# Optimization experiments

Hardware: AMD Instinct MI355X
Metric: run time of the kernel (lower is better)

Reference implementation:

```python
import jax, jax.numpy as jnp
import numpy as np

B, C, D, H, W = 4, 64, 64, 64, 64
EPS = 1e-5

def setup_inputs() -> dict:
    key = jax.random.key(0)
    ks = jax.random.split(key, 10)
    s = 1.0 / np.sqrt(C)
    so = 1.0 / np.sqrt(D)
    return {
        "x": jax.random.normal(ks[0], (B, C, H, W), jnp.float32),
        "gn_weight": jnp.ones((C,), jnp.float32),
        "gn_bias": jnp.zeros((C,), jnp.float32),
        "wq": jax.random.uniform(ks[1], (D, C), jnp.float32, -s, s),
        "bq": jax.random.uniform(ks[2], (D,), jnp.float32, -s, s),
        "wk": jax.random.uniform(ks[3], (D, C), jnp.float32, -s, s),
        "bk": jax.random.uniform(ks[4], (D,), jnp.float32, -s, s),
        "wv": jax.random.uniform(ks[5], (D, C), jnp.float32, -s, s),
        "bv": jax.random.uniform(ks[6], (D,), jnp.float32, -s, s),
        "wo": jax.random.uniform(ks[7], (D, D), jnp.float32, -so, so),
        "bo": jax.random.uniform(ks[8], (D,), jnp.float32, -so, so),
    }

def reference(x, gn_weight, gn_bias, wq, bq, wk, bk, wv, bv, wo, bo):
    # GroupNorm with num_groups == channels: per (batch, channel) norm over H,W
    mu = jnp.mean(x, axis=(2, 3), keepdims=True)
    var = jnp.var(x, axis=(2, 3), keepdims=True)
    xn = (x - mu) * jax.lax.rsqrt(var + EPS)
    xn = xn * gn_weight[None, :, None, None] + gn_bias[None, :, None, None]

    # 1x1 convs == channel matmuls; flatten spatial: bcn
    xf = xn.reshape(B, C, H * W)
    Q = jnp.einsum('dc,bcn->bdn', wq, xf) + bq[None, :, None]
    K = jnp.einsum('dc,bcn->bdn', wk, xf) + bk[None, :, None]
    V = jnp.einsum('dc,bcn->bdn', wv, xf) + bv[None, :, None]

    scale = 1.0 / jnp.sqrt(jnp.asarray(D, x.dtype))
    aff = jnp.einsum('bdn,bdm->bnm', Q, K) * scale  # [B, N, N]
    aff = jax.nn.softmax(aff, axis=2)
    att = jnp.einsum('bnm,bdm->bdn', aff, V)  # [B, D, N]

    out = jnp.einsum('ed,bdn->ben', wo, att) + bo[None, :, None]
    return out.reshape(B, D, H, W)
```

## Files before the change

kernel.cpp:

```cpp
#include <hip/hip_runtime.h>


#define B_ 4
#define C_ 64
#define D_ 64
#define N_ 4096

using bf16x8 = __attribute__((ext_vector_type(8))) short;
using u16x8  = __attribute__((ext_vector_type(8))) unsigned short;
using u32x4  = __attribute__((ext_vector_type(4))) unsigned int;
using f32x16 = __attribute__((ext_vector_type(16))) float;
using h16x8  = __attribute__((ext_vector_type(8))) _Float16;

__device__ __forceinline__ unsigned short f2bf(float f) {
    unsigned u = __builtin_bit_cast(unsigned, f);
    u = (u + 0x7FFFu + ((u >> 16) & 1u)) >> 16;
    return (unsigned short)u;
}

__device__ __forceinline__ void gload16(const void* g, void* l) {
    __builtin_amdgcn_global_load_lds(
        (const __attribute__((address_space(1))) unsigned int*)g,
        (__attribute__((address_space(3))) unsigned int*)l, 16, 0, 0);
}

__global__ __launch_bounds__(1024)
void gn_stats_kernel(const float* __restrict__ x, float* __restrict__ stats) {
    __shared__ float red[32];
    const int bx  = blockIdx.x;
    const int tid = threadIdx.x;
    const float4* xp = (const float4*)(x + (size_t)bx * N_);
    float4 v = xp[tid];
    float s = (v.x + v.y) + (v.z + v.w);
    float q = (v.x * v.x + v.y * v.y) + (v.z * v.z + v.w * v.w);
#pragma unroll
    for (int off = 1; off < 64; off <<= 1) {
        s += __shfl_xor(s, off);
        q += __shfl_xor(q, off);
    }
    const int w = tid >> 6;
    if ((tid & 63) == 0) { red[w * 2] = s; red[w * 2 + 1] = q; }
    __syncthreads();
    if (w == 0) {
        const int lane = tid & 63;
        float sl = (lane < 16) ? red[lane * 2] : 0.f;
        float ql = (lane < 16) ? red[lane * 2 + 1] : 0.f;
#pragma unroll
        for (int off = 1; off < 16; off <<= 1) {
            sl += __shfl_xor(sl, off);
            ql += __shfl_xor(ql, off);
        }
        if (lane == 0) {
            float mu  = sl * (1.f / 4096.f);
            float var = ql * (1.f / 4096.f) - mu * mu;
            var = fmaxf(var, 0.f);
            stats[bx * 2]     = mu;
            stats[bx * 2 + 1] = 1.f / sqrtf(var + 1e-5f);
        }
    }
}

__global__ __launch_bounds__(512)
void gn_qkv_kernel(const float* __restrict__ x, const float* __restrict__ stats,
                   const float* __restrict__ gnw, const float* __restrict__ gnb,
                   const float* __restrict__ wq, const float* __restrict__ bq,
                   const float* __restrict__ wk, const float* __restrict__ bk,
                   const float* __restrict__ wv, const float* __restrict__ bv,
                   unsigned short* __restrict__ Qt, unsigned short* __restrict__ Kf,
                   unsigned short* __restrict__ Vf) {
    __shared__ float xn[64 * 64];
    __shared__ __align__(16) char vs[64 * 128];
    const int t  = threadIdx.x;
    const int bx = blockIdx.x;
    const int b  = bx >> 6;
    const int n0 = (bx & 63) * 64;

    {
        const int c  = t >> 3;
        const int nc = (t & 7) * 8;
        const float* xp = x + (size_t)(b * 64 + c) * N_ + n0 + nc;
        float4 xa = *(const float4*)(xp);
        float4 xb = *(const float4*)(xp + 4);
        float mu = stats[(b * 64 + c) * 2];
        float rs = stats[(b * 64 + c) * 2 + 1];
        float gw = gnw[c] * rs;
        float gb = gnb[c] - mu * gw;
        float* xr = xn + c * 64 + nc;
        xr[0] = xa.x * gw + gb; xr[1] = xa.y * gw + gb;
        xr[2] = xa.z * gw + gb; xr[3] = xa.w * gw + gb;
        xr[4] = xb.x * gw + gb; xr[5] = xb.y * gw + gb;
        xr[6] = xb.z * gw + gb; xr[7] = xb.w * gw + gb;
    }
    __syncthreads();

    const int n    = t & 63;
    const int dblk = __builtin_amdgcn_readfirstlane(t >> 6);
    const int d0   = dblk * 8;

    float aq[8], ak[8], av[8];
#pragma unroll
    for (int i = 0; i < 8; ++i) { aq[i] = 0.f; ak[i] = 0.f; av[i] = 0.f; }

#pragma unroll 4
    for (int c = 0; c < 64; ++c) {
        const float xv = xn[c * 64 + n];
#pragma unroll
        for (int i = 0; i < 8; ++i) {
            aq[i] += wq[(d0 + i) * 64 + c] * xv;
            ak[i] += wk[(d0 + i) * 64 + c] * xv;
            av[i] += wv[(d0 + i) * 64 + c] * xv;
        }
    }

    const float QS = 0.18033688011112042f;
    const int m = n0 + n;
    u16x8 qv, kv, vb;
#pragma unroll
    for (int i = 0; i < 8; ++i) {
        qv[i] = f2bf((aq[i] + bq[d0 + i]) * QS);
        kv[i] = f2bf(ak[i] + bk[d0 + i]);
        vb[i] = f2bf(av[i] + bv[d0 + i]);
    }
    *(u16x8*)(Qt + ((size_t)(b * N_ + m)) * 64 + d0) = qv;
    {
        const int kc = dblk >> 1, h = dblk & 1, mt = m >> 5;
        *(u16x8*)(Kf + ((size_t)((b * 128 + mt) * 4 + kc)) * 512
                     + (h * 32 + (m & 31)) * 8) = kv;
    }
    *(u16x8*)(vs + n * 128 + ((dblk * 16) ^ ((n & 7) << 4))) = vb;
    __syncthreads();

    {
        const int mc_l = t >> 7;
        const int dt   = (t >> 6) & 1;
        const int lp   = t & 63;
        const int hp   = lp >> 5;
        const int dcol = (lp & 31) + dt * 32;
        const int cbase = (dcol & ~7) * 2;
        const int clow  = (dcol & 7) * 2;
        u16x8 tmp;
#pragma unroll
        for (int j = 0; j < 8; ++j) {
            const int ml = mc_l * 16 + hp * 8 + j;
            tmp[j] = *(const unsigned short*)(
                vs + ml * 128 + (cbase ^ (j << 4)) + clow);
        }
        *(u16x8*)(Vf + ((size_t)((b * 256 + (n0 >> 4) + mc_l) * 2 + dt)) * 512
                     + lp * 8) = tmp;
    }
}

__global__ __launch_bounds__(256, 4)
void attn_kernel(const unsigned short* __restrict__ Qt,
                 const unsigned short* __restrict__ Kf,
                 const unsigned short* __restrict__ Vf,
                 _Float16* __restrict__ Opart, float* __restrict__ Lpart,
                 int mspan) {
    __shared__ __align__(16) char smem[2 * 16384];
    const int tid  = threadIdx.x;
    const int lane = tid & 63;
    const int wvu  = __builtin_amdgcn_readfirstlane(tid >> 6);
    const int c    = lane & 31;
    const int h    = lane >> 5;
    const int bid  = blockIdx.x;
    const int b    = bid & 3;
    const int t2   = bid >> 2;
    const int qb   = t2 & 31;
    const int s    = t2 >> 5;
    const int qg0  = qb * 128 + wvu * 32;

    const unsigned short* qp = Qt + (size_t)(b * N_ + qg0 + c) * 64 + h * 8;
    bf16x8 qa[4];
#pragma unroll
    for (int kc = 0; kc < 4; ++kc) qa[kc] = *(const bf16x8*)(qp + kc * 16);

    f32x16 oacc0, oacc1;
#pragma unroll
    for (int i = 0; i < 16; ++i) { oacc0[i] = 0.f; oacc1[i] = 0.f; }
    float lsum = 0.f;

    const char* kfB = (const char*)Kf + (size_t)b * 524288;
    const char* vfB = (const char*)Vf + (size_t)b * 524288;
    const int   lof = lane * 16;

    const int NT = mspan >> 6;
    const int mstart = s * mspan;

    {
        const char* kT = kfB + (size_t)(mstart >> 5) * 4096;
        const char* vT = vfB + (size_t)(mstart >> 4) * 2048;
        gload16(kT + (wvu    ) * 1024 + lof, smem + (wvu    ) * 1024);
        gload16(kT + (wvu + 4) * 1024 + lof, smem + (wvu + 4) * 1024);
        gload16(vT + (wvu    ) * 1024 + lof, smem + 8192 + (wvu    ) * 1024);
        gload16(vT + (wvu + 4) * 1024 + lof, smem + 8192 + (wvu + 4) * 1024);
    }
    __syncthreads();

    for (int t = 0; t < NT; ++t) {
        char* buf = smem + ((t & 1) ? 16384 : 0);
        if (t + 1 < NT) {
            const int mn = mstart + (t + 1) * 64;
            const char* kT = kfB + (size_t)(mn >> 5) * 4096;
            const char* vT = vfB + (size_t)(mn >> 4) * 2048;
            char* dst = smem + ((t & 1) ? 0 : 16384);
            gload16(kT + (wvu    ) * 1024 + lof, dst + (wvu    ) * 1024);
            gload16(kT + (wvu + 4) * 1024 + lof, dst + (wvu + 4) * 1024);
            gload16(vT + (wvu    ) * 1024 + lof, dst + 8192 + (wvu    ) * 1024);
            gload16(vT + (wvu + 4) * 1024 + lof, dst + 8192 + (wvu + 4) * 1024);
        }

#pragma unroll
        for (int g = 0; g < 2; ++g) {
            const char* kb = buf + g * 4096 + lof;
            bf16x8 kf0 = *(const bf16x8*)(kb);
            bf16x8 kf1 = *(const bf16x8*)(kb + 1024);
            bf16x8 kf2 = *(const bf16x8*)(kb + 2048);
            bf16x8 kf3 = *(const bf16x8*)(kb + 3072);
            f32x16 sa;
#pragma unroll
            for (int i = 0; i < 16; ++i) sa[i] = 0.f;
            __builtin_amdgcn_s_setprio(1);
            sa = __builtin_amdgcn_mfma_f32_32x32x16_bf16(kf0, qa[0], sa, 0, 0, 0);
            sa = __builtin_amdgcn_mfma_f32_32x32x16_bf16(kf1, qa[1], sa, 0, 0, 0);
            sa = __builtin_amdgcn_mfma_f32_32x32x16_bf16(kf2, qa[2], sa, 0, 0, 0);
            sa = __builtin_amdgcn_mfma_f32_32x32x16_bf16(kf3, qa[3], sa, 0, 0, 0);
            __builtin_amdgcn_s_setprio(0);
#pragma unroll
            for (int i = 0; i < 16; ++i) {
                float pv = exp2f(sa[i]);
                sa[i] = pv;
                lsum += pv;
            }
            unsigned dw[8];
#pragma unroll
            for (int i = 0; i < 8; ++i)
                asm("v_cvt_pk_bf16_f32 %0, %1, %2"
                    : "=v"(dw[i]) : "v"(sa[2 * i]), "v"(sa[2 * i + 1]));
            asm("v_permlane32_swap_b32 %0, %1" : "+v"(dw[0]), "+v"(dw[2]));
            asm("v_permlane32_swap_b32 %0, %1" : "+v"(dw[1]), "+v"(dw[3]));
            asm("v_permlane32_swap_b32 %0, %1" : "+v"(dw[4]), "+v"(dw[6]));
            asm("v_permlane32_swap_b32 %0, %1" : "+v"(dw[5]), "+v"(dw[7]));
            bf16x8 pf0 = __builtin_bit_cast(bf16x8, (u32x4){dw[0], dw[1], dw[2], dw[3]});
            bf16x8 pf1 = __builtin_bit_cast(bf16x8, (u32x4){dw[4], dw[5], dw[6], dw[7]});

            const char* vb = buf + 8192 + g * 4096 + lof;
            bf16x8 vf0 = *(const bf16x8*)(vb);
            bf16x8 vf1 = *(const bf16x8*)(vb + 1024);
            bf16x8 vf2 = *(const bf16x8*)(vb + 2048);
            bf16x8 vf3 = *(const bf16x8*)(vb + 3072);
            __builtin_amdgcn_s_setprio(1);
            oacc0 = __builtin_amdgcn_mfma_f32_32x32x16_bf16(vf0, pf0, oacc0, 0, 0, 0);
            oacc1 = __builtin_amdgcn_mfma_f32_32x32x16_bf16(vf1, pf0, oacc1, 0, 0, 0);
            oacc0 = __builtin_amdgcn_mfma_f32_32x32x16_bf16(vf2, pf1, oacc0, 0, 0, 0);
            oacc1 = __builtin_amdgcn_mfma_f32_32x32x16_bf16(vf3, pf1, oacc1, 0, 0, 0);
            __builtin_amdgcn_s_setprio(0);
        }

        __syncthreads();
    }

    float rs = lsum + __shfl_xor(lsum, 32);

    const size_t s4b = (size_t)(s * 4 + b);
    _Float16* ob = Opart + (s4b * 64 << 12);
#pragma unroll
    for (int r = 0; r < 16; ++r) {
        const int row = (r & 3) + 8 * (r >> 2) + 4 * h;
        ob[((size_t)row << 12) + qg0 + c]        = (_Float16)oacc0[r];
        ob[((size_t)(row + 32) << 12) + qg0 + c] = (_Float16)oacc1[r];
    }
    if (h == 0)
        Lpart[(s4b << 12) + qg0 + c] = rs;
}

__global__ __launch_bounds__(256)
void out_proj_kernel(const _Float16* __restrict__ Opart, const float* __restrict__ Lpart,
                     const float* __restrict__ wo, const float* __restrict__ bo,
                     float* __restrict__ out, int S) {
    __shared__ float invl[32];
    __shared__ float attm[64 * 33];
    const int t  = threadIdx.x;
    const int bx = blockIdx.x;
    const int b  = bx >> 7;
    const int n0 = (bx & 127) * 32;

    if (t < 32) {
        float sum = 0.f;
        for (int s = 0; s < S; ++s)
            sum += Lpart[(((size_t)(s * 4 + b)) << 12) + n0 + t];
        invl[t] = 1.f / sum;
    }
    __syncthreads();

    {
        const int d  = t >> 2;
        const int nb = (t & 3) * 8;
        float o[8] = {0.f, 0.f, 0.f, 0.f, 0.f, 0.f, 0.f, 0.f};
        for (int s = 0; s < S; ++s) {
            h16x8 v = *(const h16x8*)(
                Opart + (((size_t)((s * 4 + b) * 64 + d)) << 12) + n0 + nb);
#pragma unroll
            for (int j = 0; j < 8; ++j) o[j] += (float)v[j];
        }
#pragma unroll
        for (int j = 0; j < 8; ++j)
            attm[d * 33 + nb + j] = o[j] * invl[nb + j];
    }
    __syncthreads();

    const int nn = t & 31;
    const int e0 = (t >> 5) * 8;
    float acc[8];
#pragma unroll
    for (int i = 0; i < 8; ++i) acc[i] = bo[e0 + i];
#pragma unroll 8
    for (int d = 0; d < 64; ++d) {
        const float xv = attm[d * 33 + nn];
#pragma unroll
        for (int i = 0; i < 8; ++i) acc[i] += wo[(e0 + i) * 64 + d] * xv;
    }
#pragma unroll
    for (int i = 0; i < 8; ++i)
        out[((size_t)(b * 64 + e0 + i) << 12) + n0 + nn] = acc[i];
}

extern "C" void kernel_launch(void* const* d_in, const int* in_sizes, int n_in,
                              void* d_out, int out_size, void* d_ws, size_t ws_size,
                              hipStream_t stream) {
    const float* x   = (const float*)d_in[0];
    const float* gnw = (const float*)d_in[1];
    const float* gnb = (const float*)d_in[2];
    const float* wq  = (const float*)d_in[3];
    const float* bq  = (const float*)d_in[4];
    const float* wk  = (const float*)d_in[5];
    const float* bk  = (const float*)d_in[6];
    const float* wv  = (const float*)d_in[7];
    const float* bv  = (const float*)d_in[8];
    const float* wo  = (const float*)d_in[9];
    const float* bo  = (const float*)d_in[10];
    float* out = (float*)d_out;

    char* wsb = (char*)d_ws;
    float*          stats = (float*)wsb;
    unsigned short* Qt    = (unsigned short*)(wsb + 2048);
    unsigned short* Kf    = (unsigned short*)(wsb + 2048 + 2097152);
    unsigned short* Vf    = (unsigned short*)(wsb + 2048 + 2 * 2097152);

    const size_t base = 2048 + 3ull * 2097152;
    auto need = [&](int S) {
        return base + (size_t)S * (65536 + 2097152);
    };
    const int S = (ws_size >= need(8)) ? 8
                : (ws_size >= need(4)) ? 4
                : (ws_size >= need(2)) ? 2 : 1;
    const int mspan = N_ / S;
    float*    Lpart = (float*)(wsb + base);
    _Float16* Opart = (_Float16*)(wsb + base + (size_t)S * 65536);

    gn_stats_kernel<<<dim3(B_ * C_), dim3(1024), 0, stream>>>(x, stats);
    gn_qkv_kernel<<<dim3(B_ * 64), dim3(512), 0, stream>>>(
        x, stats, gnw, gnb, wq, bq, wk, bk, wv, bv, Qt, Kf, Vf);
    attn_kernel<<<dim3(128 * S), dim3(256), 0, stream>>>(
        Qt, Kf, Vf, Opart, Lpart, mspan);
    out_proj_kernel<<<dim3(B_ * 128), dim3(256), 0, stream>>>(
        Opart, Lpart, wo, bo, out, S);
}
```

Measured before the change: 69.73 us.

## Fuse all four stages into one persistent cooperative kernel with grid syncs

Replaces the four separate launches (GN stats, GN+QKV projection, attention, output projection) with a single cooperative persistent kernel. Each phase loops over virtual blocks and is separated from the next by grid.sync(). The QKV stage is retiled to 16-column chunks with float4 weight loads so that it fits 256 threads. This removes launch gaps and inter-kernel drains, at the cost of grid-barrier overhead, smaller QKV tiles and occupancy tied to the attention phase's resource needs.

```diff
diff --git a/kernel.cpp b/kernel.cpp
--- a/kernel.cpp
+++ b/kernel.cpp
@@ -1,4 +1,7 @@
 #include <hip/hip_runtime.h>
+#include <hip/hip_cooperative_groups.h>
+
+namespace cg = cooperative_groups;
 
 
 #define B_ 4
@@ -7,6 +10,7 @@
 #define N_ 4096
 
 using bf16x8 = __attribute__((ext_vector_type(8))) short;
+using u16x4  = __attribute__((ext_vector_type(4))) unsigned short;
 using u16x8  = __attribute__((ext_vector_type(8))) unsigned short;
 using u32x4  = __attribute__((ext_vector_type(4))) unsigned int;
 using f32x16 = __attribute__((ext_vector_type(16))) float;
@@ -24,304 +28,306 @@
         (__attribute__((address_space(3))) unsigned int*)l, 16, 0, 0);
 }
 
-__global__ __launch_bounds__(1024)
-void gn_stats_kernel(const float* __restrict__ x, float* __restrict__ stats) {
-    __shared__ float red[32];
-    const int bx  = blockIdx.x;
+__global__ __launch_bounds__(256, 4)
+void fused_kernel(const float* __restrict__ x, const float* __restrict__ gnw,
+                  const float* __restrict__ gnb, const float* __restrict__ wq,
+                  const float* __restrict__ bq, const float* __restrict__ wk,
+                  const float* __restrict__ bk, const float* __restrict__ wv,
+                  const float* __restrict__ bv, const float* __restrict__ wo,
+                  const float* __restrict__ bo, float* __restrict__ out,
+                  float* __restrict__ stats, unsigned short* __restrict__ Qt,
+                  unsigned short* __restrict__ Kf, unsigned short* __restrict__ Vf,
+                  _Float16* __restrict__ Opart, float* __restrict__ Lpart,
+                  int S, int mspan) {
+    __shared__ __align__(16) char smem[32768];
+    cg::grid_group grid = cg::this_grid();
     const int tid = threadIdx.x;
-    const float4* xp = (const float4*)(x + (size_t)bx * N_);
-    float4 v = xp[tid];
-    float s = (v.x + v.y) + (v.z + v.w);
-    float q = (v.x * v.x + v.y * v.y) + (v.z * v.z + v.w * v.w);
-#pragma unroll
-    for (int off = 1; off < 64; off <<= 1) {
-        s += __shfl_xor(s, off);
-        q += __shfl_xor(q, off);
-    }
-    const int w = tid >> 6;
-    if ((tid & 63) == 0) { red[w * 2] = s; red[w * 2 + 1] = q; }
-    __syncthreads();
-    if (w == 0) {
-        const int lane = tid & 63;
-        float sl = (lane < 16) ? red[lane * 2] : 0.f;
-        float ql = (lane < 16) ? red[lane * 2 + 1] : 0.f;
-#pragma unroll
-        for (int off = 1; off < 16; off <<= 1) {
-            sl += __shfl_xor(sl, off);
-            ql += __shfl_xor(ql, off);
-        }
-        if (lane == 0) {
-            float mu  = sl * (1.f / 4096.f);
-            float var = ql * (1.f / 4096.f) - mu * mu;
-            var = fmaxf(var, 0.f);
-            stats[bx * 2]     = mu;
-            stats[bx * 2 + 1] = 1.f / sqrtf(var + 1e-5f);
+    const int G   = gridDim.x;
+    const int bid = blockIdx.x;
+
+    {
+        float* red = (float*)smem;
+        for (int vb = bid; vb < B_ * C_; vb += G) {
+            const float4* xp = (const float4*)(x + (size_t)vb * N_);
+            float s = 0.f, q = 0.f;
+#pragma unroll
+            for (int r = 0; r < 4; ++r) {
+                float4 v = xp[r * 256 + tid];
+                s += (v.x + v.y) + (v.z + v.w);
+                q += (v.x * v.x + v.y * v.y) + (v.z * v.z + v.w * v.w);
+            }
+#pragma unroll
+            for (int off = 1; off < 64; off <<= 1) {
+                s += __shfl_xor(s, off);
+                q += __shfl_xor(q, off);
+            }
+            const int w = tid >> 6;
+            if ((tid & 63) == 0) { red[w * 2] = s; red[w * 2 + 1] = q; }
+            __syncthreads();
+            if (tid == 0) {
+                float Sm = red[0] + red[2] + red[4] + red[6];
+                float Qm = red[1] + red[3] + red[5] + red[7];
+                float mu  = Sm * (1.f / 4096.f);
+                float var = Qm * (1.f / 4096.f) - mu * mu;
+                var = fmaxf(var, 0.f);
+                stats[vb * 2]     = mu;
+                stats[vb * 2 + 1] = 1.f / sqrtf(var + 1e-5f);
+            }
+            __syncthreads();
         }
     }
-}
-
-__global__ __launch_bounds__(512)
-void gn_qkv_kernel(const float* __restrict__ x, const float* __restrict__ stats,
-                   const float* __restrict__ gnw, const float* __restrict__ gnb,
-                   const float* __restrict__ wq, const float* __restrict__ bq,
-                   const float* __restrict__ wk, const float* __restrict__ bk,
-                   const float* __restrict__ wv, const float* __restrict__ bv,
-                   unsigned short* __restrict__ Qt, unsigned short* __restrict__ Kf,
-                   unsigned short* __restrict__ Vf) {
-    __shared__ float xn[64 * 64];
-    __shared__ __align__(16) char vs[64 * 128];
-    const int t  = threadIdx.x;
-    const int bx = blockIdx.x;
-    const int b  = bx >> 6;
-    const int n0 = (bx & 63) * 64;
+    grid.sync();
 
     {
-        const int c  = t >> 3;
-        const int nc = (t & 7) * 8;
-        const float* xp = x + (size_t)(b * 64 + c) * N_ + n0 + nc;
-        float4 xa = *(const float4*)(xp);
-        float4 xb = *(const float4*)(xp + 4);
-        float mu = stats[(b * 64 + c) * 2];
-        float rs = stats[(b * 64 + c) * 2 + 1];
-        float gw = gnw[c] * rs;
-        float gb = gnb[c] - mu * gw;
-        float* xr = xn + c * 64 + nc;
-        xr[0] = xa.x * gw + gb; xr[1] = xa.y * gw + gb;
-        xr[2] = xa.z * gw + gb; xr[3] = xa.w * gw + gb;
-        xr[4] = xb.x * gw + gb; xr[5] = xb.y * gw + gb;
-        xr[6] = xb.z * gw + gb; xr[7] = xb.w * gw + gb;
-    }
-    __syncthreads();
-
-    const int n    = t & 63;
-    const int dblk = __builtin_amdgcn_readfirstlane(t >> 6);
-    const int d0   = dblk * 8;
-
-    float aq[8], ak[8], av[8];
-#pragma unroll
-    for (int i = 0; i < 8; ++i) { aq[i] = 0.f; ak[i] = 0.f; av[i] = 0.f; }
-
+        float* xn = (float*)smem;
+        char*  vs = smem + 4096;
+        for (int vb = bid; vb < 1024; vb += G) {
+            const int b  = vb >> 8;
+            const int n0 = (vb & 255) * 16;
+            {
+                const int c = tid >> 2;
+                const int j = (tid & 3) * 4;
+                float4 xv = *(const float4*)(x + (size_t)(b * 64 + c) * N_ + n0 + j);
+                float mu = stats[(b * 64 + c) * 2];
+                float rs = stats[(b * 64 + c) * 2 + 1];
+                float gw = gnw[c] * rs;
+                float gb = gnb[c] - mu * gw;
+                xn[c * 16 + j + 0] = xv.x * gw + gb;
+                xn[c * 16 + j + 1] = xv.y * gw + gb;
+                xn[c * 16 + j + 2] = xv.z * gw + gb;
+                xn[c * 16 + j + 3] = xv.w * gw + gb;
+            }
+            __syncthreads();
+
+            const int n  = tid & 15;
+            const int d0 = (tid >> 4) * 4;
+            float aq[4] = {0.f, 0.f, 0.f, 0.f};
+            float ak[4] = {0.f, 0.f, 0.f, 0.f};
+            float av[4] = {0.f, 0.f, 0.f, 0.f};
 #pragma unroll 4
-    for (int c = 0; c < 64; ++c) {
-        const float xv = xn[c * 64 + n];
-#pragma unroll
-        for (int i = 0; i < 8; ++i) {
-            aq[i] += wq[(d0 + i) * 64 + c] * xv;
-            ak[i] += wk[(d0 + i) * 64 + c] * xv;
-            av[i] += wv[(d0 + i) * 64 + c] * xv;
+            for (int c4 = 0; c4 < 16; ++c4) {
+                float x0 = xn[(c4 * 4 + 0) * 16 + n];
+                float x1 = xn[(c4 * 4 + 1) * 16 + n];
+                float x2 = xn[(c4 * 4 + 2) * 16 + n];
+                float x3 = xn[(c4 * 4 + 3) * 16 + n];
+#pragma unroll
+                for (int i = 0; i < 4; ++i) {
+                    float4 wq4 = *(const float4*)(wq + (d0 + i) * 64 + c4 * 4);
+                    float4 wk4 = *(const float4*)(wk + (d0 + i) * 64 + c4 * 4);
+                    float4 wv4 = *(const float4*)(wv + (d0 + i) * 64 + c4 * 4);
+                    aq[i] += wq4.x * x0 + wq4.y * x1 + wq4.z * x2 + wq4.w * x3;
+                    ak[i] += wk4.x * x0 + wk4.y * x1 + wk4.z * x2 + wk4.w * x3;
+                    av[i] += wv4.x * x0 + wv4.y * x1 + wv4.z * x2 + wv4.w * x3;
+                }
+            }
+
+            const float QS = 0.18033688011112042f;
+            const int m = n0 + n;
+            u16x4 qv, kv, vv;
+#pragma unroll
+            for (int i = 0; i < 4; ++i) {
+                qv[i] = f2bf((aq[i] + bq[d0 + i]) * QS);
+                kv[i] = f2bf(ak[i] + bk[d0 + i]);
+                vv[i] = f2bf(av[i] + bv[d0 + i]);
+            }
+            *(u16x4*)(Qt + (size_t)(b * N_ + m) * 64 + d0) = qv;
+            {
+                const int kc = d0 >> 4, hk = (d0 >> 3) & 1, mt = m >> 5;
+                *(u16x4*)(Kf + ((size_t)((b * 128 + mt) * 4 + kc)) * 512
+                             + (hk * 32 + (m & 31)) * 8 + (d0 & 7)) = kv;
+            }
+            *(u16x4*)(vs + n * 128 + (((d0 >> 3) * 16) ^ ((n & 7) << 4))
+                         + (d0 & 7) * 2) = vv;
+            __syncthreads();
+
+            if (tid < 128) {
+                const int dt = tid >> 6;
+                const int lp = tid & 63;
+                const int hp = lp >> 5;
+                const int dcol  = (lp & 31) + dt * 32;
+                const int cbase = (dcol & ~7) * 2;
+                const int clow  = (dcol & 7) * 2;
+                u16x8 tmp;
+#pragma unroll
+                for (int j = 0; j < 8; ++j)
+                    tmp[j] = *(const unsigned short*)(
+                        vs + (hp * 8 + j) * 128 + (cbase ^ (j << 4)) + clow);
+                *(u16x8*)(Vf + ((size_t)((b * 256 + (n0 >> 4)) * 2 + dt)) * 512
+                             + lp * 8) = tmp;
+            }
+            __syncthreads();
         }
     }
-
-    const float QS = 0.18033688011112042f;
-    const int m = n0 + n;
-    u16x8 qv, kv, vb;
-#pragma unroll
-    for (int i = 0; i < 8; ++i) {
-        qv[i] = f2bf((aq[i] + bq[d0 + i]) * QS);
-        kv[i] = f2bf(ak[i] + bk[d0 + i]);
-        vb[i] = f2bf(av[i] + bv[d0 + i]);
+    grid.sync();
+
+    {
+        char* abuf = smem;
+        const int lane = tid & 63;
+        const int wvu  = __builtin_amdgcn_readfirstlane(tid >> 6);
+        const int c    = lane & 31;
+        const int h    = lane >> 5;
+        const int lof  = lane * 16;
+        const int nvb  = 128 * S;
+
+        for (int vb = bid; vb < nvb; vb += G) {
+            const int b   = vb & 3;
+            const int t2  = vb >> 2;
+            const int qb  = t2 & 31;
+            const int s   = t2 >> 5;
+            const int qg0 = qb * 128 + wvu * 32;
+
+            const unsigned short* qp = Qt + (size_t)(b * N_ + qg0 + c) * 64 + h * 8;
+            bf16x8 qa[4];
+#pragma unroll
+            for (int kc = 0; kc < 4; ++kc) qa[kc] = *(const bf16x8*)(qp + kc * 16);
+
+            f32x16 oacc0, oacc1;
+#pragma unroll
+            for (int i = 0; i < 16; ++i) { oacc0[i] = 0.f; oacc1[i] = 0.f; }
+            float lsum = 0.f;
+
+            const char* kfB = (const char*)Kf + (size_t)b * 524288;
+            const char* vfB = (const char*)Vf + (size_t)b * 524288;
+            const int NT = mspan >> 6;
+            const int mstart = s * mspan;
+
+            {
+                const char* kT = kfB + (size_t)(mstart >> 5) * 4096;
+                const char* vT = vfB + (size_t)(mstart >> 4) * 2048;
+                gload16(kT + (wvu    ) * 1024 + lof, abuf + (wvu    ) * 1024);
+                gload16(kT + (wvu + 4) * 1024 + lof, abuf + (wvu + 4) * 1024);
+                gload16(vT + (wvu    ) * 1024 + lof, abuf + 8192 + (wvu    ) * 1024);
+                gload16(vT + (wvu + 4) * 1024 + lof, abuf + 8192 + (wvu + 4) * 1024);
+            }
+            __syncthreads();
+
+            for (int t = 0; t < NT; ++t) {
+                char* buf = abuf + ((t & 1) ? 16384 : 0);
+                if (t + 1 < NT) {
+                    const int mn = mstart + (t + 1) * 64;
+                    const char* kT = kfB + (size_t)(mn >> 5) * 4096;
+                    const char* vT = vfB + (size_t)(mn >> 4) * 2048;
+                    char* dst = abuf + ((t & 1) ? 0 : 16384);
+                    gload16(kT + (wvu    ) * 1024 + lof, dst + (wvu    ) * 1024);
+                    gload16(kT + (wvu + 4) * 1024 + lof, dst + (wvu + 4) * 1024);
+                    gload16(vT + (wvu    ) * 1024 + lof, dst + 8192 + (wvu    ) * 1024);
+                    gload16(vT + (wvu + 4) * 1024 + lof, dst + 8192 + (wvu + 4) * 1024);
+                }
+
+#pragma unroll
+                for (int g = 0; g < 2; ++g) {
+                    const char* kb = buf + g * 4096 + lof;
+                    bf16x8 kf0 = *(const bf16x8*)(kb);
+                    bf16x8 kf1 = *(const bf16x8*)(kb + 1024);
+                    bf16x8 kf2 = *(const bf16x8*)(kb + 2048);
+                    bf16x8 kf3 = *(const bf16x8*)(kb + 3072);
+                    f32x16 sa;
+#pragma unroll
+                    for (int i = 0; i < 16; ++i) sa[i] = 0.f;
+                    __builtin_amdgcn_s_setprio(1);
+                    sa = __builtin_amdgcn_mfma_f32_32x32x16_bf16(kf0, qa[0], sa, 0, 0, 0);
+                    sa = __builtin_amdgcn_mfma_f32_32x32x16_bf16(kf1, qa[1], sa, 0, 0, 0);
+                    sa = __builtin_amdgcn_mfma_f32_32x32x16_bf16(kf2, qa[2], sa, 0, 0, 0);
+                    sa = __builtin_amdgcn_mfma_f32_32x32x16_bf16(kf3, qa[3], sa, 0, 0, 0);
+                    __builtin_amdgcn_s_setprio(0);
+#pragma unroll
+                    for (int i = 0; i < 16; ++i) {
+                        float pv = exp2f(sa[i]);
+                        sa[i] = pv;
+                        lsum += pv;
+                    }
+                    unsigned dw[8];
+#pragma unroll
+                    for (int i = 0; i < 8; ++i)
+                        asm("v_cvt_pk_bf16_f32 %0, %1, %2"
+                            : "=v"(dw[i]) : "v"(sa[2 * i]), "v"(sa[2 * i + 1]));
+                    asm("v_permlane32_swap_b32 %0, %1" : "+v"(dw[0]), "+v"(dw[2]));
+                    asm("v_permlane32_swap_b32 %0, %1" : "+v"(dw[1]), "+v"(dw[3]));
+                    asm("v_permlane32_swap_b32 %0, %1" : "+v"(dw[4]), "+v"(dw[6]));
+                    asm("v_permlane32_swap_b32 %0, %1" : "+v"(dw[5]), "+v"(dw[7]));
+                    bf16x8 pf0 = __builtin_bit_cast(bf16x8, (u32x4){dw[0], dw[1], dw[2], dw[3]});
+                    bf16x8 pf1 = __builtin_bit_cast(bf16x8, (u32x4){dw[4], dw[5], dw[6], dw[7]});
+
+                    const char* vbp = buf + 8192 + g * 4096 + lof;
+                    bf16x8 vf0 = *(const bf16x8*)(vbp);
+                    bf16x8 vf1 = *(const bf16x8*)(vbp + 1024);
+                    bf16x8 vf2 = *(const bf16x8*)(vbp + 2048);
+                    bf16x8 vf3 = *(const bf16x8*)(vbp + 3072);
+                    __builtin_amdgcn_s_setprio(1);
+                    oacc0 = __builtin_amdgcn_mfma_f32_32x32x16_bf16(vf0, pf0, oacc0, 0, 0, 0);
+                    oacc1 = __builtin_amdgcn_mfma_f32_32x32x16_bf16(vf1, pf0, oacc1, 0, 0, 0);
+                    oacc0 = __builtin_amdgcn_mfma_f32_32x32x16_bf16(vf2, pf1, oacc0, 0, 0, 0);
+                    oacc1 = __builtin_amdgcn_mfma_f32_32x32x16_bf16(vf3, pf1, oacc1, 0, 0, 0);
+                    __builtin_amdgcn_s_setprio(0);
+                }
+                __syncthreads();
+            }
+
+            float rs = lsum + __shfl_xor(lsum, 32);
+            const size_t s4b = (size_t)(s * 4 + b);
+            _Float16* ob = Opart + (s4b * 64 << 12);
+#pragma unroll
+            for (int r = 0; r < 16; ++r) {
+                const int row = (r & 3) + 8 * (r >> 2) + 4 * h;
+                ob[((size_t)row << 12) + qg0 + c]        = (_Float16)oacc0[r];
+                ob[((size_t)(row + 32) << 12) + qg0 + c] = (_Float16)oacc1[r];
+            }
+            if (h == 0)
+                Lpart[(s4b << 12) + qg0 + c] = rs;
+        }
     }
-    *(u16x8*)(Qt + ((size_t)(b * N_ + m)) * 64 + d0) = qv;
+    grid.sync();
+
     {
-        const int kc = dblk >> 1, h = dblk & 1, mt = m >> 5;
-        *(u16x8*)(Kf + ((size_t)((b * 128 + mt) * 4 + kc)) * 512
-                     + (h * 32 + (m & 31)) * 8) = kv;
+        float* invl = (float*)smem;
+        float* attm = (float*)(smem + 128);
+        for (int vb = bid; vb < 512; vb += G) {
+            const int b  = vb >> 7;
+            const int n0 = (vb & 127) * 32;
+
+            if (tid < 32) {
+                float sum = 0.f;
+                for (int s = 0; s < S; ++s)
+                    sum += Lpart[(((size_t)(s * 4 + b)) << 12) + n0 + tid];
+                invl[tid] = 1.f / sum;
+            }
+            __syncthreads();
+
+            {
+                const int d  = tid >> 2;
+                const int nb = (tid & 3) * 8;
+                float o[8] = {0.f, 0.f, 0.f, 0.f, 0.f, 0.f, 0.f, 0.f};
+                for (int s = 0; s < S; ++s) {
+                    h16x8 v = *(const h16x8*)(
+                        Opart + (((size_t)((s * 4 + b) * 64 + d)) << 12) + n0 + nb);
+#pragma unroll
+                    for (int j = 0; j < 8; ++j) o[j] += (float)v[j];
+                }
+#pragma unroll
+                for (int j = 0; j < 8; ++j)
+                    attm[d * 33 + nb + j] = o[j] * invl[nb + j];
+            }
+            __syncthreads();
+
+            {
+                const int nn = tid & 31;
+                const int e0 = (tid >> 5) * 8;
+                float acc[8];
+#pragma unroll
+                for (int i = 0; i < 8; ++i) acc[i] = bo[e0 + i];
+#pragma unroll 8
+                for (int d = 0; d < 64; ++d) {
+                    const float xv = attm[d * 33 + nn];
+#pragma unroll
+                    for (int i = 0; i < 8; ++i) acc[i] += wo[(e0 + i) * 64 + d] * xv;
+                }
+#pragma unroll
+                for (int i = 0; i < 8; ++i)
+                    out[((size_t)(b * 64 + e0 + i) << 12) + n0 + nn] = acc[i];
+            }
+            __syncthreads();
+        }
     }
-    *(u16x8*)(vs + n * 128 + ((dblk * 16) ^ ((n & 7) << 4))) = vb;
-    __syncthreads();
-
-    {
-        const int mc_l = t >> 7;
-        const int dt   = (t >> 6) & 1;
-        const int lp   = t & 63;
-        const int hp   = lp >> 5;
-        const int dcol = (lp & 31) + dt * 32;
-        const int cbase = (dcol & ~7) * 2;
-        const int clow  = (dcol & 7) * 2;
-        u16x8 tmp;
-#pragma unroll
-        for (int j = 0; j < 8; ++j) {
-            const int ml = mc_l * 16 + hp * 8 + j;
-            tmp[j] = *(const unsigned short*)(
-                vs + ml * 128 + (cbase ^ (j << 4)) + clow);
-        }
-        *(u16x8*)(Vf + ((size_t)((b * 256 + (n0 >> 4) + mc_l) * 2 + dt)) * 512
-                     + lp * 8) = tmp;
-    }
-}
-
-__global__ __launch_bounds__(256, 4)
-void attn_kernel(const unsigned short* __restrict__ Qt,
-                 const unsigned short* __restrict__ Kf,
-                 const unsigned short* __restrict__ Vf,
-                 _Float16* __restrict__ Opart, float* __restrict__ Lpart,
-                 int mspan) {
-    __shared__ __align__(16) char smem[2 * 16384];
-    const int tid  = threadIdx.x;
-    const int lane = tid & 63;
-    const int wvu  = __builtin_amdgcn_readfirstlane(tid >> 6);
-    const int c    = lane & 31;
-    const int h    = lane >> 5;
-    const int bid  = blockIdx.x;
-    const int b    = bid & 3;
-    const int t2   = bid >> 2;
-    const int qb   = t2 & 31;
-    const int s    = t2 >> 5;
-    const int qg0  = qb * 128 + wvu * 32;
-
-    const unsigned short* qp = Qt + (size_t)(b * N_ + qg0 + c) * 64 + h * 8;
-    bf16x8 qa[4];
-#pragma unroll
-    for (int kc = 0; kc < 4; ++kc) qa[kc] = *(const bf16x8*)(qp + kc * 16);
-
-    f32x16 oacc0, oacc1;
-#pragma unroll
-    for (int i = 0; i < 16; ++i) { oacc0[i] = 0.f; oacc1[i] = 0.f; }
-    float lsum = 0.f;
-
-    const char* kfB = (const char*)Kf + (size_t)b * 524288;
-    const char* vfB = (const char*)Vf + (size_t)b * 524288;
-    const int   lof = lane * 16;
-
-    const int NT = mspan >> 6;
-    const int mstart = s * mspan;
-
-    {
-        const char* kT = kfB + (size_t)(mstart >> 5) * 4096;
-        const char* vT = vfB + (size_t)(mstart >> 4) * 2048;
-        gload16(kT + (wvu    ) * 1024 + lof, smem + (wvu    ) * 1024);
-        gload16(kT + (wvu + 4) * 1024 + lof, smem + (wvu + 4) * 1024);
-        gload16(vT + (wvu    ) * 1024 + lof, smem + 8192 + (wvu    ) * 1024);
-        gload16(vT + (wvu + 4) * 1024 + lof, smem + 8192 + (wvu + 4) * 1024);
-    }
-    __syncthreads();
-
-    for (int t = 0; t < NT; ++t) {
-        char* buf = smem + ((t & 1) ? 16384 : 0);
-        if (t + 1 < NT) {
-            const int mn = mstart + (t + 1) * 64;
-            const char* kT = kfB + (size_t)(mn >> 5) * 4096;
-            const char* vT = vfB + (size_t)(mn >> 4) * 2048;
-            char* dst = smem + ((t & 1) ? 0 : 16384);
-            gload16(kT + (wvu    ) * 1024 + lof, dst + (wvu    ) * 1024);
-            gload16(kT + (wvu + 4) * 1024 + lof, dst + (wvu + 4) * 1024);
-            gload16(vT + (wvu    ) * 1024 + lof, dst + 8192 + (wvu    ) * 1024);
-            gload16(vT + (wvu + 4) * 1024 + lof, dst + 8192 + (wvu + 4) * 1024);
-        }
-
-#pragma unroll
-        for (int g = 0; g < 2; ++g) {
-            const char* kb = buf + g * 4096 + lof;
-            bf16x8 kf0 = *(const bf16x8*)(kb);
-            bf16x8 kf1 = *(const bf16x8*)(kb + 1024);
-            bf16x8 kf2 = *(const bf16x8*)(kb + 2048);
-            bf16x8 kf3 = *(const bf16x8*)(kb + 3072);
-            f32x16 sa;
-#pragma unroll
-            for (int i = 0; i < 16; ++i) sa[i] = 0.f;
-            __builtin_amdgcn_s_setprio(1);
-            sa = __builtin_amdgcn_mfma_f32_32x32x16_bf16(kf0, qa[0], sa, 0, 0, 0);
-            sa = __builtin_amdgcn_mfma_f32_32x32x16_bf16(kf1, qa[1], sa, 0, 0, 0);
-            sa = __builtin_amdgcn_mfma_f32_32x32x16_bf16(kf2, qa[2], sa, 0, 0, 0);
-            sa = __builtin_amdgcn_mfma_f32_32x32x16_bf16(kf3, qa[3], sa, 0, 0, 0);
-            __builtin_amdgcn_s_setprio(0);
-#pragma unroll
-            for (int i = 0; i < 16; ++i) {
-                float pv = exp2f(sa[i]);
-                sa[i] = pv;
-                lsum += pv;
-            }
-            unsigned dw[8];
-#pragma unroll
-            for (int i = 0; i < 8; ++i)
-                asm("v_cvt_pk_bf16_f32 %0, %1, %2"
-                    : "=v"(dw[i]) : "v"(sa[2 * i]), "v"(sa[2 * i + 1]));
-            asm("v_permlane32_swap_b32 %0, %1" : "+v"(dw[0]), "+v"(dw[2]));
-            asm("v_permlane32_swap_b32 %0, %1" : "+v"(dw[1]), "+v"(dw[3]));
-            asm("v_permlane32_swap_b32 %0, %1" : "+v"(dw[4]), "+v"(dw[6]));
-            asm("v_permlane32_swap_b32 %0, %1" : "+v"(dw[5]), "+v"(dw[7]));
-            bf16x8 pf0 = __builtin_bit_cast(bf16x8, (u32x4){dw[0], dw[1], dw[2], dw[3]});
-            bf16x8 pf1 = __builtin_bit_cast(bf16x8, (u32x4){dw[4], dw[5], dw[6], dw[7]});
-
-            const char* vb = buf + 8192 + g * 4096 + lof;
-            bf16x8 vf0 = *(const bf16x8*)(vb);
-            bf16x8 vf1 = *(const bf16x8*)(vb + 1024);
-            bf16x8 vf2 = *(const bf16x8*)(vb + 2048);
-            bf16x8 vf3 = *(const bf16x8*)(vb + 3072);
-            __builtin_amdgcn_s_setprio(1);
-            oacc0 = __builtin_amdgcn_mfma_f32_32x32x16_bf16(vf0, pf0, oacc0, 0, 0, 0);
-            oacc1 = __builtin_amdgcn_mfma_f32_32x32x16_bf16(vf1, pf0, oacc1, 0, 0, 0);
-            oacc0 = __builtin_amdgcn_mfma_f32_32x32x16_bf16(vf2, pf1, oacc0, 0, 0, 0);
-            oacc1 = __builtin_amdgcn_mfma_f32_32x32x16_bf16(vf3, pf1, oacc1, 0, 0, 0);
-            __builtin_amdgcn_s_setprio(0);
-        }
-
-        __syncthreads();
-    }
-
-    float rs = lsum + __shfl_xor(lsum, 32);
-
-    const size_t s4b = (size_t)(s * 4 + b);
-    _Float16* ob = Opart + (s4b * 64 << 12);
-#pragma unroll
-    for (int r = 0; r < 16; ++r) {
-        const int row = (r & 3) + 8 * (r >> 2) + 4 * h;
-        ob[((size_t)row << 12) + qg0 + c]        = (_Float16)oacc0[r];
-        ob[((size_t)(row + 32) << 12) + qg0 + c] = (_Float16)oacc1[r];
-    }
-    if (h == 0)
-        Lpart[(s4b << 12) + qg0 + c] = rs;
-}
-
-__global__ __launch_bounds__(256)
-void out_proj_kernel(const _Float16* __restrict__ Opart, const float* __restrict__ Lpart,
-                     const float* __restrict__ wo, const float* __restrict__ bo,
-                     float* __restrict__ out, int S) {
-    __shared__ float invl[32];
-    __shared__ float attm[64 * 33];
-    const int t  = threadIdx.x;
-    const int bx = blockIdx.x;
-    const int b  = bx >> 7;
-    const int n0 = (bx & 127) * 32;
-
-    if (t < 32) {
-        float sum = 0.f;
-        for (int s = 0; s < S; ++s)
-            sum += Lpart[(((size_t)(s * 4 + b)) << 12) + n0 + t];
-        invl[t] = 1.f / sum;
-    }
-    __syncthreads();
-
-    {
-        const int d  = t >> 2;
-        const int nb = (t & 3) * 8;
-        float o[8] = {0.f, 0.f, 0.f, 0.f, 0.f, 0.f, 0.f, 0.f};
-        for (int s = 0; s < S; ++s) {
-            h16x8 v = *(const h16x8*)(
-                Opart + (((size_t)((s * 4 + b) * 64 + d)) << 12) + n0 + nb);
-#pragma unroll
-            for (int j = 0; j < 8; ++j) o[j] += (float)v[j];
-        }
-#pragma unroll
-        for (int j = 0; j < 8; ++j)
-            attm[d * 33 + nb + j] = o[j] * invl[nb + j];
-    }
-    __syncthreads();
-
-    const int nn = t & 31;
-    const int e0 = (t >> 5) * 8;
-    float acc[8];
-#pragma unroll
-    for (int i = 0; i < 8; ++i) acc[i] = bo[e0 + i];
-#pragma unroll 8
-    for (int d = 0; d < 64; ++d) {
-        const float xv = attm[d * 33 + nn];
-#pragma unroll
-        for (int i = 0; i < 8; ++i) acc[i] += wo[(e0 + i) * 64 + d] * xv;
-    }
-#pragma unroll
-    for (int i = 0; i < 8; ++i)
-        out[((size_t)(b * 64 + e0 + i) << 12) + n0 + nn] = acc[i];
 }
 
 extern "C" void kernel_launch(void* const* d_in, const int* in_sizes, int n_in,
@@ -347,21 +353,29 @@
     unsigned short* Vf    = (unsigned short*)(wsb + 2048 + 2 * 2097152);
 
     const size_t base = 2048 + 3ull * 2097152;
-    auto need = [&](int S) {
-        return base + (size_t)S * (65536 + 2097152);
+    auto need = [&](int s) {
+        return base + (size_t)s * (65536 + 2097152);
     };
-    const int S = (ws_size >= need(8)) ? 8
-                : (ws_size >= need(4)) ? 4
-                : (ws_size >= need(2)) ? 2 : 1;
-    const int mspan = N_ / S;
+    int S = (ws_size >= need(8)) ? 8
+          : (ws_size >= need(4)) ? 4
+          : (ws_size >= need(2)) ? 2 : 1;
+    int mspan = N_ / S;
     float*    Lpart = (float*)(wsb + base);
     _Float16* Opart = (_Float16*)(wsb + base + (size_t)S * 65536);
 
-    gn_stats_kernel<<<dim3(B_ * C_), dim3(1024), 0, stream>>>(x, stats);
-    gn_qkv_kernel<<<dim3(B_ * 64), dim3(512), 0, stream>>>(
-        x, stats, gnw, gnb, wq, bq, wk, bk, wv, bv, Qt, Kf, Vf);
-    attn_kernel<<<dim3(128 * S), dim3(256), 0, stream>>>(
-        Qt, Kf, Vf, Opart, Lpart, mspan);
-    out_proj_kernel<<<dim3(B_ * 128), dim3(256), 0, stream>>>(
-        Opart, Lpart, wo, bo, out, S);
+    int perCU = 0;
+    if (hipOccupancyMaxActiveBlocksPerMultiprocessor(
+            &perCU, (const void*)fused_kernel, 256, 0) != hipSuccess || perCU < 1)
+        perCU = 1;
+    int G = perCU * 256;
+    if (G > 1024) G = 1024;
+
+    void* args[] = {
+        (void*)&x, (void*)&gnw, (void*)&gnb, (void*)&wq, (void*)&bq,
+        (void*)&wk, (void*)&bk, (void*)&wv, (void*)&bv, (void*)&wo,
+        (void*)&bo, (void*)&out, (void*)&stats, (void*)&Qt, (void*)&Kf,
+        (void*)&Vf, (void*)&Opart, (void*)&Lpart, (void*)&S, (void*)&mspan,
+    };
+    hipLaunchCooperativeKernel((const void*)fused_kernel, dim3(G), dim3(256),
+                               args, 0, stream);
 }
```

Measured after the change: 250.9 us. 3.6x slower.
